# Performance work log

Measured on AMD Instinct MI355X. Metric: run time of the kernel, lower is better.

Reference implementation:

```python
import jax, jax.numpy as jnp
import numpy as np

H, W = 256, 256          # detector height/width (pixels)
DELX, DELY = 2.0, 2.0    # detector pixel pitch (mm)
EPS = 1e-8


def _rot(theta, phi, gamma):
    """R = Rz(theta) @ Ry(phi) @ Rx(gamma)."""
    ct, st = jnp.cos(theta), jnp.sin(theta)
    cp, sp = jnp.cos(phi), jnp.sin(phi)
    cg, sg = jnp.cos(gamma), jnp.sin(gamma)
    one = jnp.ones_like(ct); zero = jnp.zeros_like(ct)
    Rz = jnp.stack([jnp.stack([ct, -st, zero]), jnp.stack([st, ct, zero]), jnp.stack([zero, zero, one])])
    Ry = jnp.stack([jnp.stack([cp, zero, sp]), jnp.stack([zero, one, zero]), jnp.stack([-sp, zero, cp])])
    Rx = jnp.stack([jnp.stack([one, zero, zero]), jnp.stack([zero, cg, -sg]), jnp.stack([zero, sg, cg])])
    return Rz @ Ry @ Rx


def _make_xrays(sdr, rotations, translations):
    """Source point (3,) and detector-plane targets (H*W, 3)."""
    R = _rot(rotations[0], rotations[1], rotations[2])
    source = sdr * R[:, 0] + translations      # (3,)
    center = -sdr * R[:, 0] + translations     # detector center, opposite side
    u, v = R[:, 1], R[:, 2]                    # detector in-plane basis (unit)
    t = (jnp.arange(-(H // 2), H // 2, dtype=jnp.float32) + 1.0) * DELX  # (H,)
    s = (jnp.arange(-(W // 2), W // 2, dtype=jnp.float32) + 1.0) * DELY  # (W,)
    # cartesian_prod(t, s) @ [u; v]  ->  t_i * u + s_j * v   (t varies slowest)
    targets = t[:, None, None] * u + s[None, :, None] * v    # (H, W, 3)
    targets = targets.reshape(-1, 3) + center                # (H*W, 3)
    return source, targets


def _raytrace(volume, spacing, source, targets):
    """Siddon ray-tracing: line integral of volume along each source->target ray."""
    nx, ny, nz = volume.shape                       # planes per axis = n + 1
    dims = jnp.array([nx + 1, ny + 1, nz + 1], dtype=jnp.float32)
    sdd = targets - source + EPS                     # (R, 3) ray direction (unnormalized)

    # Entry/exit parametric range [alphamin, alphamax] per ray
    a0 = (0.0 * spacing - source) / sdd              # alpha at first planes
    a1 = ((dims - 1.0) * spacing - source) / sdd     # alpha at last planes
    amin = jnp.max(jnp.minimum(a0, a1), axis=-1, keepdims=True)  # (R, 1)
    amax = jnp.min(jnp.maximum(a0, a1), axis=-1, keepdims=True)  # (R, 1)

    # Alphas at every axis-aligned plane intersection
    ax = (jnp.arange(nx + 1, dtype=jnp.float32) * spacing[0] - source[0]) / sdd[:, 0:1]
    ay = (jnp.arange(ny + 1, dtype=jnp.float32) * spacing[1] - source[1]) / sdd[:, 1:2]
    az = (jnp.arange(nz + 1, dtype=jnp.float32) * spacing[2] - source[2]) / sdd[:, 2:3]
    alphas = jnp.concatenate([ax, ay, az], axis=-1)  # (R, P) with P = nx+ny+nz+3

    # Out-of-range alphas -> amax (amax is itself a kept plane intersection, so the
    # extra trailing segments have zero length; equivalent to the torch NaN trick
    # but NaN-free, so gradients stay clean).
    good = (alphas >= amin) & (alphas <= amax)
    alphas = jnp.where(good, alphas, amax)
    alphas = jnp.sort(alphas, axis=-1)

    amid = 0.5 * (alphas[:, :-1] + alphas[:, 1:])    # (R, P-1) segment midpoints
    step = jnp.diff(alphas, axis=-1)                 # (R, P-1) segment lengths (alpha units)

    # Voxel containing each midpoint (trunc == floor for in-volume points)
    pts = source + amid[..., None] * sdd[:, None, :] # (R, P-1, 3)
    idx = jnp.trunc(pts / spacing).astype(jnp.int32)
    idx = jnp.clip(idx, 0, jnp.array([nx - 1, ny - 1, nz - 1], dtype=jnp.int32))
    vox = volume[idx[..., 0], idx[..., 1], idx[..., 2]]  # (R, P-1)

    drr = jnp.sum(vox * step, axis=-1)               # (R,)
    raylength = jnp.linalg.norm(sdd, axis=-1)        # convert alpha units -> mm
    return drr * raylength


def setup_inputs() -> dict:
    key = jax.random.key(0)
    volume = jax.random.uniform(key, (256, 256, 256), dtype=jnp.float32)  # CT attenuation
    spacing = jnp.ones((3,), dtype=jnp.float32)
    sdr = jnp.asarray(300.0, dtype=jnp.float32)
    rotations = jnp.array([np.pi, 0.0, np.pi / 2], dtype=jnp.float32)     # theta, phi, gamma
    translations = jnp.array([128.0, 128.0, 128.0], dtype=jnp.float32)    # volume center
    return {"volume": volume, "spacing": spacing, "sdr": sdr,
            "rotations": rotations, "translations": translations}


def reference(volume, spacing, sdr, rotations, translations):
    source, targets = _make_xrays(sdr, rotations, translations)
    return _raytrace(volume, spacing, source, targets)  # (H*W,)
```

## Files before the change

### kernel.cpp

```cpp
#include <hip/hip_runtime.h>
#include <math.h>


#define NPLANE 256
constexpr int TPR = 16;

__device__ __forceinline__ float palpha(int i, float sp, float src, float rd) {
    return fmaf((float)i, sp, -src) * rd;
}

__global__ __launch_bounds__(256) void drr_kernel(
    const float* __restrict__ vol,
    const float* __restrict__ spacing,
    const float* __restrict__ sdrp,
    const float* __restrict__ rot,
    const float* __restrict__ trans,
    float* __restrict__ out)
{
    int tid  = threadIdx.x;
    int part = tid >> 4;
    int rlo  = tid & 15;
    int rl   = ((int)blockIdx.x << 4) | rlo;

    float theta = rot[0], phi = rot[1], gam = rot[2];
    float ct = cosf(theta), st = sinf(theta);
    float cp = cosf(phi),   sp_ = sinf(phi);
    float cg = cosf(gam),   sg = sinf(gam);

    float r0x = ct * cp, r0y = st * cp, r0z = -sp_;
    float ux = ct * sp_ * sg - st * cg, uy = st * sp_ * sg + ct * cg, uz = cp * sg;
    float vx = ct * sp_ * cg + st * sg, vy = st * sp_ * cg - ct * sg, vz = cp * cg;

    float cost_u = fabsf(ux) * 65536.f + fabsf(uy) * 256.f + fabsf(uz);
    float cost_v = fabsf(vx) * 65536.f + fabsf(vy) * 256.f + fabsf(vz);
    bool tfast = cost_u < cost_v;
    int ti = tfast ? (rl & 255) : (rl >> 8);
    int si = tfast ? (rl >> 8) : (rl & 255);

    float sdr = sdrp[0];
    float tx = trans[0], ty = trans[1], tz = trans[2];

    float sx = sdr * r0x + tx,  sy = sdr * r0y + ty,  sz = sdr * r0z + tz;
    float cxx = -sdr * r0x + tx, cxy = -sdr * r0y + ty, cxz = -sdr * r0z + tz;

    float tval = (float)(ti - 127) * 2.0f;
    float sval = (float)(si - 127) * 2.0f;

    float gx = tval * ux + sval * vx + cxx;
    float gy = tval * uy + sval * vy + cxy;
    float gz = tval * uz + sval * vz + cxz;

    float sdx = gx - sx + 1e-8f;
    float sdy = gy - sy + 1e-8f;
    float sdz = gz - sz + 1e-8f;

    float spx = spacing[0], spy = spacing[1], spz = spacing[2];
    float rdx = 1.0f / sdx, rdy = 1.0f / sdy, rdz = 1.0f / sdz;

    float a0x = palpha(0, spx, sx, rdx), a1x = palpha(NPLANE, spx, sx, rdx);
    float a0y = palpha(0, spy, sy, rdy), a1y = palpha(NPLANE, spy, sy, rdy);
    float a0z = palpha(0, spz, sz, rdz), a1z = palpha(NPLANE, spz, sz, rdz);

    float amin = fmaxf(fmaxf(fminf(a0x, a1x), fminf(a0y, a1y)), fminf(a0z, a1z));
    float amax = fminf(fminf(fmaxf(a0x, a1x), fmaxf(a0y, a1y)), fmaxf(a0z, a1z));

    float acc = 0.f;

    if (amax > amin) {
        float range = amax - amin;
        constexpr float inv = 1.0f / (float)TPR;
        float lo = fmaf(range, (float)part * inv, amin);
        float hi = (part == TPR - 1) ? INFINITY
                                     : fmaf(range, (float)(part + 1) * inv, amin);
        float end = fminf(hi, amax);

        int ix, iy, iz, dix, diy, diz;
        float nxx, nxy, nxz;

        #define SETUP(SP, SRC, SDD, RD, I, DI, NXT)                                \
        {                                                                          \
            float q = fmaf(lo, SDD, SRC) / (SP);                                   \
            q = fminf(fmaxf(q, -1.f), 257.f);                                      \
            if ((SDD) > 0.f) {                                                     \
                DI = 1;                                                            \
                I = (int)ceilf(q);                                                 \
                while (I > 0 && palpha(I - 1, SP, SRC, RD) >= lo) --I;             \
                while (I <= NPLANE && palpha(I, SP, SRC, RD) < lo) ++I;            \
                NXT = (I <= NPLANE) ? palpha(I, SP, SRC, RD) : INFINITY;           \
            } else {                                                               \
                DI = -1;                                                           \
                I = (int)floorf(q);                                                \
                while (I < NPLANE && palpha(I + 1, SP, SRC, RD) >= lo) ++I;        \
                while (I >= 0 && palpha(I, SP, SRC, RD) < lo) --I;                 \
                NXT = (I >= 0) ? palpha(I, SP, SRC, RD) : INFINITY;                \
            }                                                                      \
        }

        SETUP(spx, sx, sdx, rdx, ix, dix, nxx)
        SETUP(spy, sy, sdy, rdy, iy, diy, nxy)
        SETUP(spz, sz, sdz, rdz, iz, diz, nxz)
        #undef SETUP

        float ispx = 1.0f / spx, ispy = 1.0f / spy, ispz = 1.0f / spz;

        #define ADVANCE_MERGE()                                                    \
            if (nxx == cur) { ix += dix;                                           \
                nxx = ((unsigned)ix <= NPLANE) ? palpha(ix, spx, sx, rdx)          \
                                               : INFINITY; }                       \
            if (nxy == cur) { iy += diy;                                           \
                nxy = ((unsigned)iy <= NPLANE) ? palpha(iy, spy, sy, rdy)          \
                                               : INFINITY; }                       \
            if (nxz == cur) { iz += diz;                                           \
                nxz = ((unsigned)iz <= NPLANE) ? palpha(iz, spz, sz, rdz)          \
                                               : INFINITY; }

        #define SEG_ADDR(CUR, E, ADDR)                                             \
        {                                                                          \
            float amid = 0.5f * ((CUR) + (E));                                     \
            float pxv = fmaf(amid, sdx, sx) * ispx;                                \
            float pyv = fmaf(amid, sdy, sy) * ispy;                                \
            float pzv = fmaf(amid, sdz, sz) * ispz;                                \
            int jx = (int)pxv; jx = jx < 0 ? 0 : (jx > 255 ? 255 : jx);            \
            int jy = (int)pyv; jy = jy < 0 ? 0 : (jy > 255 ? 255 : jy);            \
            int jz = (int)pzv; jz = jz < 0 ? 0 : (jz > 255 ? 255 : jz);            \
            ADDR = (jx << 16) + (jy << 8) + jz;                                    \
        }

        float cur = fminf(fminf(nxx, nxy), nxz);

        if (cur < end) {
            ADVANCE_MERGE();
            float nxt = fminf(fminf(nxx, nxy), nxz);
            float e   = fminf(nxt, amax);
            int addr; SEG_ADDR(cur, e, addr)
            float pstep = e - cur;
            float pval  = vol[addr];
            cur = nxt;

            while (cur < end) {
                ADVANCE_MERGE();
                nxt = fminf(fminf(nxx, nxy), nxz);
                e   = fminf(nxt, amax);
                int addr2; SEG_ADDR(cur, e, addr2)
                float nval = vol[addr2];
                acc = fmaf(pval, pstep, acc);
                pval  = nval;
                pstep = e - cur;
                cur = nxt;
            }
            acc = fmaf(pval, pstep, acc);
        }
        #undef ADVANCE_MERGE
        #undef SEG_ADDR
    }

    acc += __shfl_xor(acc, 16);
    acc += __shfl_xor(acc, 32);

    __shared__ float red[64];
    int wave = tid >> 6;
    if ((tid & 63) < 16)
        red[(wave << 4) | rlo] = acc;
    __syncthreads();

    if (tid < 16) {
        float s = red[tid] + red[16 + tid] + red[32 + tid] + red[48 + tid];
        float rl2 = sqrtf(sdx * sdx + sdy * sdy + sdz * sdz);
        out[ti * 256 + si] = s * rl2;
    }
}

extern "C" void kernel_launch(void* const* d_in, const int* in_sizes, int n_in,
                              void* d_out, int out_size, void* d_ws, size_t ws_size,
                              hipStream_t stream) {
    const float* vol     = (const float*)d_in[0];
    const float* spacing = (const float*)d_in[1];
    const float* sdr     = (const float*)d_in[2];
    const float* rot     = (const float*)d_in[3];
    const float* trans   = (const float*)d_in[4];
    float* out = (float*)d_out;

    int nblocks = 256 * 256 / 16;
    drr_kernel<<<nblocks, 256, 0, stream>>>(vol, spacing, sdr, rot, trans, out);
}
```

Baseline: 60.01 us.

## Remap threads so each wave handles 64 rays, split segments across two blocks

Work is remapped so each wave covers 64 consecutive rays, with each thread tracing two of the 16 ray segments. Each ray's 16 segments are split across two blocks, and the per-block partial sums are combined with atomicAdd into an output zeroed by a memset. The intent is to make lanes in a wave trace neighbouring rays, which should give more coherent memory access and less divergence. It also drops the cross-lane shuffle reduction. In exchange it adds atomics, a memset launch, and a serial two-segment loop per thread.

```diff
diff --git a/kernel.cpp b/kernel.cpp
--- a/kernel.cpp
+++ b/kernel.cpp
@@ -18,9 +18,12 @@
     float* __restrict__ out)
 {
     int tid  = threadIdx.x;
-    int part = tid >> 4;
-    int rlo  = tid & 15;
-    int rl   = ((int)blockIdx.x << 4) | rlo;
+    int lane = tid & 63;
+    int wave = tid >> 6;
+    int b    = blockIdx.x;
+    int g    = b >> 1;
+    int j    = b & 1;
+    int rl   = (g << 6) | lane;
 
     float theta = rot[0], phi = rot[1], gam = rot[2];
     float ct = cosf(theta), st = sinf(theta);
@@ -64,109 +67,112 @@
     float amin = fmaxf(fmaxf(fminf(a0x, a1x), fminf(a0y, a1y)), fminf(a0z, a1z));
     float amax = fminf(fminf(fmaxf(a0x, a1x), fmaxf(a0y, a1y)), fmaxf(a0z, a1z));
 
-    float acc = 0.f;
+    float accT = 0.f;
 
     if (amax > amin) {
         float range = amax - amin;
         constexpr float inv = 1.0f / (float)TPR;
-        float lo = fmaf(range, (float)part * inv, amin);
-        float hi = (part == TPR - 1) ? INFINITY
-                                     : fmaf(range, (float)(part + 1) * inv, amin);
-        float end = fminf(hi, amax);
-
-        int ix, iy, iz, dix, diy, diz;
-        float nxx, nxy, nxz;
-
-        #define SETUP(SP, SRC, SDD, RD, I, DI, NXT)                                \
-        {                                                                          \
-            float q = fmaf(lo, SDD, SRC) / (SP);                                   \
-            q = fminf(fmaxf(q, -1.f), 257.f);                                      \
-            if ((SDD) > 0.f) {                                                     \
-                DI = 1;                                                            \
-                I = (int)ceilf(q);                                                 \
-                while (I > 0 && palpha(I - 1, SP, SRC, RD) >= lo) --I;             \
-                while (I <= NPLANE && palpha(I, SP, SRC, RD) < lo) ++I;            \
-                NXT = (I <= NPLANE) ? palpha(I, SP, SRC, RD) : INFINITY;           \
-            } else {                                                               \
-                DI = -1;                                                           \
-                I = (int)floorf(q);                                                \
-                while (I < NPLANE && palpha(I + 1, SP, SRC, RD) >= lo) ++I;        \
-                while (I >= 0 && palpha(I, SP, SRC, RD) < lo) --I;                 \
-                NXT = (I >= 0) ? palpha(I, SP, SRC, RD) : INFINITY;                \
-            }                                                                      \
-        }
-
-        SETUP(spx, sx, sdx, rdx, ix, dix, nxx)
-        SETUP(spy, sy, sdy, rdy, iy, diy, nxy)
-        SETUP(spz, sz, sdz, rdz, iz, diz, nxz)
-        #undef SETUP
-
         float ispx = 1.0f / spx, ispy = 1.0f / spy, ispz = 1.0f / spz;
 
-        #define ADVANCE_MERGE()                                                    \
-            if (nxx == cur) { ix += dix;                                           \
-                nxx = ((unsigned)ix <= NPLANE) ? palpha(ix, spx, sx, rdx)          \
-                                               : INFINITY; }                       \
-            if (nxy == cur) { iy += diy;                                           \
-                nxy = ((unsigned)iy <= NPLANE) ? palpha(iy, spy, sy, rdy)          \
-                                               : INFINITY; }                       \
-            if (nxz == cur) { iz += diz;                                           \
-                nxz = ((unsigned)iz <= NPLANE) ? palpha(iz, spz, sz, rdz)          \
-                                               : INFINITY; }
+        #pragma unroll
+        for (int k = 0; k < 2; ++k) {
+            int part = 8 * j + wave + 4 * k;
+            float lo = fmaf(range, (float)part * inv, amin);
+            float hi = (part == TPR - 1) ? INFINITY
+                                         : fmaf(range, (float)(part + 1) * inv, amin);
+            float end = fminf(hi, amax);
 
-        #define SEG_ADDR(CUR, E, ADDR)                                             \
-        {                                                                          \
-            float amid = 0.5f * ((CUR) + (E));                                     \
-            float pxv = fmaf(amid, sdx, sx) * ispx;                                \
-            float pyv = fmaf(amid, sdy, sy) * ispy;                                \
-            float pzv = fmaf(amid, sdz, sz) * ispz;                                \
-            int jx = (int)pxv; jx = jx < 0 ? 0 : (jx > 255 ? 255 : jx);            \
-            int jy = (int)pyv; jy = jy < 0 ? 0 : (jy > 255 ? 255 : jy);            \
-            int jz = (int)pzv; jz = jz < 0 ? 0 : (jz > 255 ? 255 : jz);            \
-            ADDR = (jx << 16) + (jy << 8) + jz;                                    \
+            int ix, iy, iz, dix, diy, diz;
+            float nxx, nxy, nxz;
+
+            #define SETUP(SP, SRC, SDD, RD, I, DI, NXT)                            \
+            {                                                                      \
+                float q = fmaf(lo, SDD, SRC) / (SP);                               \
+                q = fminf(fmaxf(q, -1.f), 257.f);                                  \
+                if ((SDD) > 0.f) {                                                 \
+                    DI = 1;                                                        \
+                    I = (int)ceilf(q);                                             \
+                    while (I > 0 && palpha(I - 1, SP, SRC, RD) >= lo) --I;         \
+                    while (I <= NPLANE && palpha(I, SP, SRC, RD) < lo) ++I;        \
+                    NXT = (I <= NPLANE) ? palpha(I, SP, SRC, RD) : INFINITY;       \
+                } else {                                                           \
+                    DI = -1;                                                       \
+                    I = (int)floorf(q);                                            \
+                    while (I < NPLANE && palpha(I + 1, SP, SRC, RD) >= lo) ++I;    \
+                    while (I >= 0 && palpha(I, SP, SRC, RD) < lo) --I;             \
+                    NXT = (I >= 0) ? palpha(I, SP, SRC, RD) : INFINITY;            \
+                }                                                                  \
+            }
+
+            SETUP(spx, sx, sdx, rdx, ix, dix, nxx)
+            SETUP(spy, sy, sdy, rdy, iy, diy, nxy)
+            SETUP(spz, sz, sdz, rdz, iz, diz, nxz)
+            #undef SETUP
+
+            #define ADVANCE_MERGE()                                                \
+                if (nxx == cur) { ix += dix;                                       \
+                    nxx = ((unsigned)ix <= NPLANE) ? palpha(ix, spx, sx, rdx)      \
+                                                   : INFINITY; }                   \
+                if (nxy == cur) { iy += diy;                                       \
+                    nxy = ((unsigned)iy <= NPLANE) ? palpha(iy, spy, sy, rdy)      \
+                                                   : INFINITY; }                   \
+                if (nxz == cur) { iz += diz;                                       \
+                    nxz = ((unsigned)iz <= NPLANE) ? palpha(iz, spz, sz, rdz)      \
+                                                   : INFINITY; }
+
+            #define SEG_ADDR(CUR, E, ADDR)                                         \
+            {                                                                      \
+                float amid = 0.5f * ((CUR) + (E));                                 \
+                float pxv = fmaf(amid, sdx, sx) * ispx;                            \
+                float pyv = fmaf(amid, sdy, sy) * ispy;                            \
+                float pzv = fmaf(amid, sdz, sz) * ispz;                            \
+                int jx = (int)pxv; jx = jx < 0 ? 0 : (jx > 255 ? 255 : jx);        \
+                int jy = (int)pyv; jy = jy < 0 ? 0 : (jy > 255 ? 255 : jy);        \
+                int jz = (int)pzv; jz = jz < 0 ? 0 : (jz > 255 ? 255 : jz);        \
+                ADDR = (jx << 16) + (jy << 8) + jz;                                \
+            }
+
+            float cur = fminf(fminf(nxx, nxy), nxz);
+            float acc = 0.f;
+
+            if (cur < end) {
+                ADVANCE_MERGE();
+                float nxt = fminf(fminf(nxx, nxy), nxz);
+                float e   = fminf(nxt, amax);
+                int addr; SEG_ADDR(cur, e, addr)
+                float pstep = e - cur;
+                float pval  = vol[addr];
+                cur = nxt;
+
+                while (cur < end) {
+                    ADVANCE_MERGE();
+                    nxt = fminf(fminf(nxx, nxy), nxz);
+                    e   = fminf(nxt, amax);
+                    int addr2; SEG_ADDR(cur, e, addr2)
+                    float nval = vol[addr2];
+                    acc = fmaf(pval, pstep, acc);
+                    pval  = nval;
+                    pstep = e - cur;
+                    cur = nxt;
+                }
+                acc = fmaf(pval, pstep, acc);
+            }
+            accT += acc;
+            #undef ADVANCE_MERGE
+            #undef SEG_ADDR
         }
-
-        float cur = fminf(fminf(nxx, nxy), nxz);
-
-        if (cur < end) {
-            ADVANCE_MERGE();
-            float nxt = fminf(fminf(nxx, nxy), nxz);
-            float e   = fminf(nxt, amax);
-            int addr; SEG_ADDR(cur, e, addr)
-            float pstep = e - cur;
-            float pval  = vol[addr];
-            cur = nxt;
-
-            while (cur < end) {
-                ADVANCE_MERGE();
-                nxt = fminf(fminf(nxx, nxy), nxz);
-                e   = fminf(nxt, amax);
-                int addr2; SEG_ADDR(cur, e, addr2)
-                float nval = vol[addr2];
-                acc = fmaf(pval, pstep, acc);
-                pval  = nval;
-                pstep = e - cur;
-                cur = nxt;
-            }
-            acc = fmaf(pval, pstep, acc);
-        }
-        #undef ADVANCE_MERGE
-        #undef SEG_ADDR
     }
 
-    acc += __shfl_xor(acc, 16);
-    acc += __shfl_xor(acc, 32);
-
-    __shared__ float red[64];
-    int wave = tid >> 6;
-    if ((tid & 63) < 16)
-        red[(wave << 4) | rlo] = acc;
+    __shared__ float red[4][64];
+    red[wave][lane] = accT;
     __syncthreads();
 
-    if (tid < 16) {
-        float s = red[tid] + red[16 + tid] + red[32 + tid] + red[48 + tid];
-        float rl2 = sqrtf(sdx * sdx + sdy * sdy + sdz * sdz);
-        out[ti * 256 + si] = s * rl2;
+    if (wave == 0) {
+        float s = red[0][lane] + red[1][lane] + red[2][lane] + red[3][lane];
+        if (s != 0.f) {
+            float rl2 = sqrtf(sdx * sdx + sdy * sdy + sdz * sdz);
+            atomicAdd(&out[ti * 256 + si], s * rl2);
+        }
     }
 }
 
@@ -180,6 +186,8 @@
     const float* trans   = (const float*)d_in[4];
     float* out = (float*)d_out;
 
-    int nblocks = 256 * 256 / 16;
+    hipMemsetAsync(out, 0, (size_t)out_size * sizeof(float), stream);
+
+    int nblocks = 2048;
     drr_kernel<<<nblocks, 256, 0, stream>>>(vol, spacing, sdr, rot, trans, out);
 }
```

New measurement: 62.24 us. 1.04x slower.

## Add x-axis fast inner loop and derive x voxel index from plane counter

Applied to the files above, without the earlier changes.

Splits the Siddon traversal into an inner loop that only steps x-plane crossings while they come before the next y/z crossing, with a general merge step otherwise. The x voxel index now comes from the integer plane counter instead of a float multiply and truncation, and the bounds checks on plane indices are dropped. This is meant to cut per-segment compare and select work along the dominant axis. In exchange it adds nested-loop divergence across lanes, the missing bounds checks rely on amax to stop traversal, and the software pipelining of loads is restructured.

```diff
diff --git a/kernel.cpp b/kernel.cpp
--- a/kernel.cpp
+++ b/kernel.cpp
@@ -101,56 +101,60 @@
         SETUP(spz, sz, sdz, rdz, iz, diz, nxz)
         #undef SETUP
 
-        float ispx = 1.0f / spx, ispy = 1.0f / spy, ispz = 1.0f / spz;
-
-        #define ADVANCE_MERGE()                                                    \
-            if (nxx == cur) { ix += dix;                                           \
-                nxx = ((unsigned)ix <= NPLANE) ? palpha(ix, spx, sx, rdx)          \
-                                               : INFINITY; }                       \
-            if (nxy == cur) { iy += diy;                                           \
-                nxy = ((unsigned)iy <= NPLANE) ? palpha(iy, spy, sy, rdy)          \
-                                               : INFINITY; }                       \
-            if (nxz == cur) { iz += diz;                                           \
-                nxz = ((unsigned)iz <= NPLANE) ? palpha(iz, spz, sz, rdz)          \
-                                               : INFINITY; }
+        float ispy = 1.0f / spy, ispz = 1.0f / spz;
+        int offcx = (dix > 0) ? -1 : 0;
 
         #define SEG_ADDR(CUR, E, ADDR)                                             \
         {                                                                          \
             float amid = 0.5f * ((CUR) + (E));                                     \
-            float pxv = fmaf(amid, sdx, sx) * ispx;                                \
             float pyv = fmaf(amid, sdy, sy) * ispy;                                \
             float pzv = fmaf(amid, sdz, sz) * ispz;                                \
-            int jx = (int)pxv; jx = jx < 0 ? 0 : (jx > 255 ? 255 : jx);            \
-            int jy = (int)pyv; jy = jy < 0 ? 0 : (jy > 255 ? 255 : jy);            \
-            int jz = (int)pzv; jz = jz < 0 ? 0 : (jz > 255 ? 255 : jz);            \
+            int jx = ix + offcx; jx = jx < 0 ? 0 : (jx > 255 ? 255 : jx);          \
+            int jy = (int)pyv;   jy = jy < 0 ? 0 : (jy > 255 ? 255 : jy);          \
+            int jz = (int)pzv;   jz = jz < 0 ? 0 : (jz > 255 ? 255 : jz);          \
             ADDR = (jx << 16) + (jy << 8) + jz;                                    \
         }
 
         float cur = fminf(fminf(nxx, nxy), nxz);
 
         if (cur < end) {
-            ADVANCE_MERGE();
-            float nxt = fminf(fminf(nxx, nxy), nxz);
-            float e   = fminf(nxt, amax);
-            int addr; SEG_ADDR(cur, e, addr)
-            float pstep = e - cur;
-            float pval  = vol[addr];
-            cur = nxt;
+            if (nxx == cur) { ix += dix; nxx = palpha(ix, spx, sx, rdx); }
+            if (nxy == cur) { iy += diy; nxy = palpha(iy, spy, sy, rdy); }
+            if (nxz == cur) { iz += diz; nxz = palpha(iz, spz, sz, rdz); }
 
             while (cur < end) {
-                ADVANCE_MERGE();
-                nxt = fminf(fminf(nxx, nxy), nxz);
-                e   = fminf(nxt, amax);
-                int addr2; SEG_ADDR(cur, e, addr2)
-                float nval = vol[addr2];
-                acc = fmaf(pval, pstep, acc);
-                pval  = nval;
-                pstep = e - cur;
+                float nyz  = fminf(nxy, nxz);
+                float rend = fminf(nyz, end);
+
+                if (nxx < rend) {
+                    float e = nxx;
+                    int addr; SEG_ADDR(cur, e, addr)
+                    float pstep = e - cur;
+                    float pval  = vol[addr];
+                    cur = e; ix += dix; nxx = palpha(ix, spx, sx, rdx);
+
+                    while (nxx < rend) {
+                        e = nxx;
+                        int addr2; SEG_ADDR(cur, e, addr2)
+                        float nval = vol[addr2];
+                        acc = fmaf(pval, pstep, acc);
+                        pval  = nval;
+                        pstep = e - cur;
+                        cur = e; ix += dix; nxx = palpha(ix, spx, sx, rdx);
+                    }
+                    acc = fmaf(pval, pstep, acc);
+                }
+
+                float nxt = fminf(nxx, nyz);
+                float e   = fminf(nxt, amax);
+                int addr; SEG_ADDR(cur, e, addr)
+                acc = fmaf(vol[addr], e - cur, acc);
                 cur = nxt;
+                if (nxx == cur) { ix += dix; nxx = palpha(ix, spx, sx, rdx); }
+                if (nxy == cur) { iy += diy; nxy = palpha(iy, spy, sy, rdy); }
+                if (nxz == cur) { iz += diz; nxz = palpha(iz, spz, sz, rdz); }
             }
-            acc = fmaf(pval, pstep, acc);
         }
-        #undef ADVANCE_MERGE
         #undef SEG_ADDR
     }
 
```

Result: slower. 68.54 us (+14.2%).

## Interleave two ray segments per thread to overlap gather latency

Applied to the files above, without the earlier changes.

Each thread now walks two independent segments of the same ray (parts q and q+8) in an interleaved loop, and the block shrinks from 256 to 128 threads. The aim is more independent volume loads in flight per thread, so gather latency is hidden by instruction-level parallelism rather than by extra threads. In exchange, register use per thread rises, and the two chains may finish at different times, leaving lanes idle under the combined loop condition.

```diff
diff --git a/kernel.cpp b/kernel.cpp
--- a/kernel.cpp
+++ b/kernel.cpp
@@ -9,7 +9,26 @@
     return fmaf((float)i, sp, -src) * rd;
 }
 
-__global__ __launch_bounds__(256) void drr_kernel(
+__device__ __forceinline__ void axis_setup(float SP, float SRC, float SDD, float RD,
+                                           float lo, int& I, int& DI, float& NXT) {
+    float q = fmaf(lo, SDD, SRC) / SP;
+    q = fminf(fmaxf(q, -1.f), 257.f);
+    if (SDD > 0.f) {
+        DI = 1;
+        I = (int)ceilf(q);
+        while (I > 0 && palpha(I - 1, SP, SRC, RD) >= lo) --I;
+        while (I <= NPLANE && palpha(I, SP, SRC, RD) < lo) ++I;
+        NXT = (I <= NPLANE) ? palpha(I, SP, SRC, RD) : INFINITY;
+    } else {
+        DI = -1;
+        I = (int)floorf(q);
+        while (I < NPLANE && palpha(I + 1, SP, SRC, RD) >= lo) ++I;
+        while (I >= 0 && palpha(I, SP, SRC, RD) < lo) --I;
+        NXT = (I >= 0) ? palpha(I, SP, SRC, RD) : INFINITY;
+    }
+}
+
+__global__ __launch_bounds__(128) void drr_kernel(
     const float* __restrict__ vol,
     const float* __restrict__ spacing,
     const float* __restrict__ sdrp,
@@ -17,10 +36,10 @@
     const float* __restrict__ trans,
     float* __restrict__ out)
 {
-    int tid  = threadIdx.x;
-    int part = tid >> 4;
-    int rlo  = tid & 15;
-    int rl   = ((int)blockIdx.x << 4) | rlo;
+    int tid = threadIdx.x;
+    int q   = tid >> 4;
+    int rlo = tid & 15;
+    int rl  = ((int)blockIdx.x << 4) | rlo;
 
     float theta = rot[0], phi = rot[1], gam = rot[2];
     float ct = cosf(theta), st = sinf(theta);
@@ -69,41 +88,41 @@
     if (amax > amin) {
         float range = amax - amin;
         constexpr float inv = 1.0f / (float)TPR;
-        float lo = fmaf(range, (float)part * inv, amin);
-        float hi = (part == TPR - 1) ? INFINITY
-                                     : fmaf(range, (float)(part + 1) * inv, amin);
-        float end = fminf(hi, amax);
+        float ispx = 1.0f / spx, ispy = 1.0f / spy, ispz = 1.0f / spz;
 
-        int ix, iy, iz, dix, diy, diz;
-        float nxx, nxy, nxz;
-
-        #define SETUP(SP, SRC, SDD, RD, I, DI, NXT)                                \
-        {                                                                          \
-            float q = fmaf(lo, SDD, SRC) / (SP);                                   \
-            q = fminf(fmaxf(q, -1.f), 257.f);                                      \
-            if ((SDD) > 0.f) {                                                     \
-                DI = 1;                                                            \
-                I = (int)ceilf(q);                                                 \
-                while (I > 0 && palpha(I - 1, SP, SRC, RD) >= lo) --I;             \
-                while (I <= NPLANE && palpha(I, SP, SRC, RD) < lo) ++I;            \
-                NXT = (I <= NPLANE) ? palpha(I, SP, SRC, RD) : INFINITY;           \
-            } else {                                                               \
-                DI = -1;                                                           \
-                I = (int)floorf(q);                                                \
-                while (I < NPLANE && palpha(I + 1, SP, SRC, RD) >= lo) ++I;        \
-                while (I >= 0 && palpha(I, SP, SRC, RD) < lo) --I;                 \
-                NXT = (I >= 0) ? palpha(I, SP, SRC, RD) : INFINITY;                \
-            }                                                                      \
+        int   ixA, iyA, izA, dixA, diyA, dizA;
+        float nxxA, nxyA, nxzA, curA, endA, pvA = 0.f, psA = 0.f;
+        {
+            int p = q;
+            float lo = fmaf(range, (float)p * inv, amin);
+            float hi = (p == TPR - 1) ? INFINITY
+                                      : fmaf(range, (float)(p + 1) * inv, amin);
+            endA = fminf(hi, amax);
+            axis_setup(spx, sx, sdx, rdx, lo, ixA, dixA, nxxA);
+            axis_setup(spy, sy, sdy, rdy, lo, iyA, diyA, nxyA);
+            axis_setup(spz, sz, sdz, rdz, lo, izA, dizA, nxzA);
+            curA = fminf(fminf(nxxA, nxyA), nxzA);
+        }
+        int   ixB, iyB, izB, dixB, diyB, dizB;
+        float nxxB, nxyB, nxzB, curB, endB, pvB = 0.f, psB = 0.f;
+        {
+            int p = q + 8;
+            float lo = fmaf(range, (float)p * inv, amin);
+            float hi = (p == TPR - 1) ? INFINITY
+                                      : fmaf(range, (float)(p + 1) * inv, amin);
+            endB = fminf(hi, amax);
+            axis_setup(spx, sx, sdx, rdx, lo, ixB, dixB, nxxB);
+            axis_setup(spy, sy, sdy, rdy, lo, iyB, diyB, nxyB);
+            axis_setup(spz, sz, sdz, rdz, lo, izB, dizB, nxzB);
+            curB = fminf(fminf(nxxB, nxyB), nxzB);
         }
 
-        SETUP(spx, sx, sdx, rdx, ix, dix, nxx)
-        SETUP(spy, sy, sdy, rdy, iy, diy, nxy)
-        SETUP(spz, sz, sdz, rdz, iz, diz, nxz)
-        #undef SETUP
+        bool actA = curA < endA;
+        bool actB = curB < endB;
 
-        float ispx = 1.0f / spx, ispy = 1.0f / spy, ispz = 1.0f / spz;
-
-        #define ADVANCE_MERGE()                                                    \
+        #define CHAIN_STEP(cur, end, nxx, nxy, nxz, ix, iy, iz, dix, diy, diz,     \
+                           pv, ps, act)                                            \
+        if (act) {                                                                 \
             if (nxx == cur) { ix += dix;                                           \
                 nxx = ((unsigned)ix <= NPLANE) ? palpha(ix, spx, sx, rdx)          \
                                                : INFINITY; }                       \
@@ -112,59 +131,46 @@
                                                : INFINITY; }                       \
             if (nxz == cur) { iz += diz;                                           \
                 nxz = ((unsigned)iz <= NPLANE) ? palpha(iz, spz, sz, rdz)          \
-                                               : INFINITY; }
-
-        #define SEG_ADDR(CUR, E, ADDR)                                             \
-        {                                                                          \
-            float amid = 0.5f * ((CUR) + (E));                                     \
+                                               : INFINITY; }                       \
+            float nxt  = fminf(fminf(nxx, nxy), nxz);                              \
+            float e    = fminf(nxt, amax);                                         \
+            float amid = 0.5f * (cur + e);                                         \
             float pxv = fmaf(amid, sdx, sx) * ispx;                                \
             float pyv = fmaf(amid, sdy, sy) * ispy;                                \
             float pzv = fmaf(amid, sdz, sz) * ispz;                                \
             int jx = (int)pxv; jx = jx < 0 ? 0 : (jx > 255 ? 255 : jx);            \
             int jy = (int)pyv; jy = jy < 0 ? 0 : (jy > 255 ? 255 : jy);            \
             int jz = (int)pzv; jz = jz < 0 ? 0 : (jz > 255 ? 255 : jz);            \
-            ADDR = (jx << 16) + (jy << 8) + jz;                                    \
+            float nv = vol[(jx << 16) + (jy << 8) + jz];                           \
+            acc = fmaf(pv, ps, acc);                                               \
+            pv = nv; ps = e - cur;                                                 \
+            cur = nxt;                                                             \
+            act = cur < end;                                                       \
         }
 
-        float cur = fminf(fminf(nxx, nxy), nxz);
+        while (actA || actB) {
+            CHAIN_STEP(curA, endA, nxxA, nxyA, nxzA, ixA, iyA, izA,
+                       dixA, diyA, dizA, pvA, psA, actA)
+            CHAIN_STEP(curB, endB, nxxB, nxyB, nxzB, ixB, iyB, izB,
+                       dixB, diyB, dizB, pvB, psB, actB)
+        }
+        #undef CHAIN_STEP
 
-        if (cur < end) {
-            ADVANCE_MERGE();
-            float nxt = fminf(fminf(nxx, nxy), nxz);
-            float e   = fminf(nxt, amax);
-            int addr; SEG_ADDR(cur, e, addr)
-            float pstep = e - cur;
-            float pval  = vol[addr];
-            cur = nxt;
-
-            while (cur < end) {
-                ADVANCE_MERGE();
-                nxt = fminf(fminf(nxx, nxy), nxz);
-                e   = fminf(nxt, amax);
-                int addr2; SEG_ADDR(cur, e, addr2)
-                float nval = vol[addr2];
-                acc = fmaf(pval, pstep, acc);
-                pval  = nval;
-                pstep = e - cur;
-                cur = nxt;
-            }
-            acc = fmaf(pval, pstep, acc);
-        }
-        #undef ADVANCE_MERGE
-        #undef SEG_ADDR
+        acc = fmaf(pvA, psA, acc);
+        acc = fmaf(pvB, psB, acc);
     }
 
     acc += __shfl_xor(acc, 16);
     acc += __shfl_xor(acc, 32);
 
-    __shared__ float red[64];
+    __shared__ float red[2][16];
     int wave = tid >> 6;
     if ((tid & 63) < 16)
-        red[(wave << 4) | rlo] = acc;
+        red[wave][rlo] = acc;
     __syncthreads();
 
     if (tid < 16) {
-        float s = red[tid] + red[16 + tid] + red[32 + tid] + red[48 + tid];
+        float s = red[0][tid] + red[1][tid];
         float rl2 = sqrtf(sdx * sdx + sdy * sdy + sdz * sdz);
         out[ti * 256 + si] = s * rl2;
     }
@@ -181,5 +187,5 @@
     float* out = (float*)d_out;
 
     int nblocks = 256 * 256 / 16;
-    drr_kernel<<<nblocks, 256, 0, stream>>>(vol, spacing, sdr, rot, trans, out);
+    drr_kernel<<<nblocks, 128, 0, stream>>>(vol, spacing, sdr, rot, trans, out);
 }
```

Result: slower. 86.49 us (+44.1%).
